# Kernel optimization log

Hardware: AMD Instinct MI355X
Metric: run time of the kernel (lower is better)

## Reference

```python
import jax, jax.numpy as jnp
import numpy as np

EMB = 1024
HID = 2048
NH = 16
NKV = 16
NE = 8
TOPK = 2
WIN = 2048
B = 2
L = 2048
HD = EMB // NH  # 64


def _layer_norm(x, g, b, eps=1e-5):
    m = jnp.mean(x, axis=-1, keepdims=True)
    v = jnp.mean((x - m) ** 2, axis=-1, keepdims=True)
    return (x - m) / jnp.sqrt(v + eps) * g + b


def setup_inputs() -> dict:
    key = jax.random.key(0)
    ks = jax.random.split(key, 12)
    w = lambda k, shape: (jax.random.normal(k, shape, jnp.float32) * 0.02)
    return {
        "x": jax.random.normal(ks[0], (B, L, EMB), jnp.float32),
        "position_idx": 0,
        "ln1_g": jnp.ones((EMB,), jnp.float32),
        "ln1_b": jnp.zeros((EMB,), jnp.float32),
        "ln2_g": jnp.ones((EMB,), jnp.float32),
        "ln2_b": jnp.zeros((EMB,), jnp.float32),
        "Wq": w(ks[1], (EMB, EMB)),
        "Wk": w(ks[2], (EMB, EMB)),
        "Wv": w(ks[3], (EMB, EMB)),
        "Wo": w(ks[4], (EMB, EMB)),
        "Wr": w(ks[5], (EMB, NE)),
        "W1": w(ks[6], (NE, EMB, HID)),
        "b1": jnp.zeros((NE, HID), jnp.float32),
        "W2": w(ks[7], (NE, HID, EMB)),
        "b2": jnp.zeros((NE, EMB), jnp.float32),
    }


def reference(x, position_idx, ln1_g, ln1_b, ln2_g, ln2_b, Wq, Wk, Wv, Wo, Wr, W1, b1, W2, b2):
    Bn, Ln, D = x.shape
    scale = 1.0 / (HD ** 0.5)

    # --- sliding-window attention (cache=None path) ---
    h = _layer_norm(x, ln1_g, ln1_b)
    q = (h @ Wq).reshape(Bn, Ln, NH, HD).transpose(0, 2, 1, 3)   # [B,H,L,hd]
    k = (h @ Wk).reshape(Bn, Ln, NKV, HD).transpose(0, 2, 1, 3)  # [B,KV,L,hd]
    v = (h @ Wv).reshape(Bn, Ln, NKV, HD).transpose(0, 2, 1, 3)
    k = k[:, :, -WIN:]
    v = v[:, :, -WIN:]
    qpk = NH // NKV
    if qpk > 1:
        k = jnp.repeat(k, qpk, axis=1)
        v = jnp.repeat(v, qpk, axis=1)
    scores = jnp.einsum('bhqd,bhkd->bhqk', q, k) * scale
    S = k.shape[2]
    i = jnp.arange(Ln)[:, None]
    j = jnp.arange(S)[None, :]
    mask = (j > i) | (j < i + position_idx - WIN)  # causal + sliding window
    scores = jnp.where(mask[None, None], -jnp.inf, scores)
    attn = jax.nn.softmax(scores, axis=-1)
    attn_out = jnp.einsum('bhqk,bhkd->bqhd', attn, v).reshape(Bn, Ln, D) @ Wo
    x = x + attn_out

    # --- top-k MoE ---
    h2 = _layer_norm(x, ln2_g, ln2_b)
    logits = h2 @ Wr                               # [B,L,E]
    top_v, top_i = jax.lax.top_k(logits, TOPK)     # [B,L,K]
    top_w = jax.nn.softmax(top_v, axis=-1)
    out = jnp.zeros_like(x)
    for e in range(NE):
        # combine weight for expert e per token (sums over top-k slots)
        we = jnp.sum(jnp.where(top_i == e, top_w, 0.0), axis=-1)  # [B,L]
        he = jax.nn.silu(h2 @ W1[e] + b1[e])
        out = out + we[..., None] * (he @ W2[e] + b2[e])
    return x + out
```

## Files before the change

### kernel.cpp

```cpp
#include <hip/hip_runtime.h>
#include <hip/hip_bf16.h>

typedef __hip_bfloat16 bf16;
typedef __attribute__((ext_vector_type(8))) short bf16x8;
typedef __attribute__((ext_vector_type(4))) float f32x4;

constexpr int kEMB = 1024;
constexpr int kHID = 2048;
constexpr int kNH  = 16;
constexpr int kNE  = 8;
constexpr int kL   = 2048;
constexpr int kHD  = 64;
constexpr int kT   = 4096;
constexpr int kSLOTS = kT * 2;
constexpr int kWIN = 2048;

__device__ __forceinline__ unsigned short f2bfbits(float f){
  bf16 h = __float2bfloat16(f);
  return __builtin_bit_cast(unsigned short, h);
}
__device__ __forceinline__ float bfbits2f(unsigned short u){
  unsigned int x = ((unsigned int)u) << 16;
  return __builtin_bit_cast(float, x);
}
__device__ __forceinline__ void gld_lds16(const void* g, void* s){
  __builtin_amdgcn_global_load_lds((const __attribute__((address_space(1))) void*)g,
                                   (__attribute__((address_space(3))) void*)s, 16, 0, 0);
}
__device__ __forceinline__ float wave_sum64(float v){
  #pragma unroll
  for (int xm = 1; xm < 64; xm <<= 1) v += __shfl_xor(v, xm, 64);
  return v;
}

__global__ __launch_bounds__(256) void tconv_k(const float* __restrict__ src, bf16* __restrict__ dst,
                                               int R, int C){
  __shared__ float tile[32][33];
  const int tx = threadIdx.x & 31, ty = threadIdx.x >> 5;
  const int bx = blockIdx.x * 32, by = blockIdx.y * 32;
  const size_t base = (size_t)blockIdx.z * R * C;
  #pragma unroll
  for (int i = 0; i < 32; i += 8)
    tile[ty + i][tx] = src[base + (size_t)(by + ty + i) * C + bx + tx];
  __syncthreads();
  #pragma unroll
  for (int i = 0; i < 32; i += 8)
    dst[base + (size_t)(bx + ty + i) * R + by + tx] = __float2bfloat16(tile[tx][ty + i]);
}

__global__ __launch_bounds__(256) void tconv4_k(const float* __restrict__ s0, const float* __restrict__ s1,
                                                const float* __restrict__ s2, const float* __restrict__ s3,
                                                bf16* __restrict__ dst){
  __shared__ float tile[32][33];
  const int tx = threadIdx.x & 31, ty = threadIdx.x >> 5;
  const int bx = blockIdx.x * 32, by = blockIdx.y * 32;
  const int z = blockIdx.z;
  const float* src = (z == 0) ? s0 : (z == 1) ? s1 : (z == 2) ? s2 : s3;
  bf16* d = dst + (size_t)z * kEMB * kEMB;
  #pragma unroll
  for (int i = 0; i < 32; i += 8)
    tile[ty + i][tx] = src[(size_t)(by + ty + i) * kEMB + bx + tx];
  __syncthreads();
  #pragma unroll
  for (int i = 0; i < 32; i += 8)
    d[(size_t)(bx + ty + i) * kEMB + by + tx] = __float2bfloat16(tile[tx][ty + i]);
}

__global__ __launch_bounds__(256) void vtrans_k(const bf16* __restrict__ v, bf16* __restrict__ vt){
  __shared__ unsigned short tile[32][33];
  const int tx = threadIdx.x & 31, ty = threadIdx.x >> 5;
  const int l0 = blockIdx.x * 32, d0 = blockIdx.y * 32;
  const unsigned short* src = (const unsigned short*)v + (size_t)blockIdx.z * kL * kHD;
  unsigned short* dst = (unsigned short*)vt + (size_t)blockIdx.z * kHD * kL;
  #pragma unroll
  for (int i = 0; i < 32; i += 8)
    tile[ty + i][tx] = src[(size_t)(l0 + ty + i) * kHD + d0 + tx];
  __syncthreads();
  #pragma unroll
  for (int i = 0; i < 32; i += 8)
    dst[(size_t)(d0 + ty + i) * kL + l0 + tx] = tile[tx][ty + i];
}

__global__ __launch_bounds__(256) void lnw_k(
    const float* __restrict__ x, const float* __restrict__ g, const float* __restrict__ bta,
    bf16* __restrict__ h)
{
  const int lane = threadIdx.x & 63, w = threadIdx.x >> 6;
  const int row = blockIdx.x * 4 + w;
  const float4* xr = (const float4*)(x + (size_t)row * kEMB);
  float4 v[4];
  #pragma unroll
  for (int j = 0; j < 4; j++) v[j] = xr[lane + 64 * j];
  float s = 0.f;
  #pragma unroll
  for (int j = 0; j < 4; j++) s += v[j].x + v[j].y + v[j].z + v[j].w;
  s = wave_sum64(s);
  const float mean = s * (1.0f / kEMB);
  float ss = 0.f;
  #pragma unroll
  for (int j = 0; j < 4; j++){
    const float a = v[j].x - mean, b = v[j].y - mean, c = v[j].z - mean, d = v[j].w - mean;
    ss += a*a + b*b + c*c + d*d;
  }
  ss = wave_sum64(ss);
  const float rstd = rsqrtf(ss * (1.0f / kEMB) + 1e-5f);
  unsigned short* hr = (unsigned short*)h + (size_t)row * kEMB;
  #pragma unroll
  for (int j = 0; j < 4; j++){
    const float4 gg = ((const float4*)g)[lane + 64 * j];
    const float4 bb = ((const float4*)bta)[lane + 64 * j];
    ushort4 pk;
    pk.x = f2bfbits((v[j].x - mean) * rstd * gg.x + bb.x);
    pk.y = f2bfbits((v[j].y - mean) * rstd * gg.y + bb.y);
    pk.z = f2bfbits((v[j].z - mean) * rstd * gg.z + bb.z);
    pk.w = f2bfbits((v[j].w - mean) * rstd * gg.w + bb.w);
    *(ushort4*)&hr[(lane + 64 * j) * 4] = pk;
  }
}

__global__ __launch_bounds__(256) void ln2w_k(
    const float* __restrict__ x, const float* __restrict__ P,
    const float* __restrict__ g, const float* __restrict__ bta,
    float* __restrict__ out, bf16* __restrict__ h, const float* __restrict__ Wr,
    int* __restrict__ top_i, float* __restrict__ top_w)
{
  const int lane = threadIdx.x & 63, w = threadIdx.x >> 6;
  const int row = blockIdx.x * 4 + w;
  const float4* xr = (const float4*)(x + (size_t)row * kEMB);
  const float4* p0 = (const float4*)(P + (size_t)row * kEMB);
  const float4* p1 = (const float4*)(P + (size_t)(kT + row) * kEMB);
  float4* outr = (float4*)(out + (size_t)row * kEMB);
  float4 v[4];
  #pragma unroll
  for (int j = 0; j < 4; j++){
    const float4 a = xr[lane + 64 * j], b = p0[lane + 64 * j], c = p1[lane + 64 * j];
    v[j].x = a.x + b.x + c.x; v[j].y = a.y + b.y + c.y;
    v[j].z = a.z + b.z + c.z; v[j].w = a.w + b.w + c.w;
    outr[lane + 64 * j] = v[j];
  }
  float s = 0.f;
  #pragma unroll
  for (int j = 0; j < 4; j++) s += v[j].x + v[j].y + v[j].z + v[j].w;
  s = wave_sum64(s);
  const float mean = s * (1.0f / kEMB);
  float ss = 0.f;
  #pragma unroll
  for (int j = 0; j < 4; j++){
    const float a = v[j].x - mean, b = v[j].y - mean, c = v[j].z - mean, d = v[j].w - mean;
    ss += a*a + b*b + c*c + d*d;
  }
  ss = wave_sum64(ss);
  const float rstd = rsqrtf(ss * (1.0f / kEMB) + 1e-5f);
  unsigned short* hr = (unsigned short*)h + (size_t)row * kEMB;
  float part[8];
  #pragma unroll
  for (int e = 0; e < 8; e++) part[e] = 0.f;
  #pragma unroll
  for (int j = 0; j < 4; j++){
    const float4 gg = ((const float4*)g)[lane + 64 * j];
    const float4 bb = ((const float4*)bta)[lane + 64 * j];
    float n[4];
    n[0] = (v[j].x - mean) * rstd * gg.x + bb.x;
    n[1] = (v[j].y - mean) * rstd * gg.y + bb.y;
    n[2] = (v[j].z - mean) * rstd * gg.z + bb.z;
    n[3] = (v[j].w - mean) * rstd * gg.w + bb.w;
    ushort4 pk;
    pk.x = f2bfbits(n[0]); pk.y = f2bfbits(n[1]); pk.z = f2bfbits(n[2]); pk.w = f2bfbits(n[3]);
    *(ushort4*)&hr[(lane + 64 * j) * 4] = pk;
    const float* wrp = Wr + (size_t)(lane + 64 * j) * 4 * kNE;
    #pragma unroll
    for (int i = 0; i < 4; i++)
      #pragma unroll
      for (int e = 0; e < 8; e++) part[e] += n[i] * wrp[i * kNE + e];
  }
  #pragma unroll
  for (int xm = 1; xm < 64; xm <<= 1)
    #pragma unroll
    for (int e = 0; e < 8; e++) part[e] += __shfl_xor(part[e], xm, 64);
  if (lane == 0){
    int i0 = 0; float v0 = part[0];
    #pragma unroll
    for (int e = 1; e < 8; e++) if (part[e] > v0){ v0 = part[e]; i0 = e; }
    int i1 = -1; float v1 = -3.4e38f;
    #pragma unroll
    for (int e = 0; e < 8; e++) if (e != i0 && part[e] > v1){ v1 = part[e]; i1 = e; }
    const float w0 = 1.0f / (1.0f + __expf(v1 - v0));
    top_i[row * 2] = i0; top_i[row * 2 + 1] = i1;
    top_w[row * 2] = w0; top_w[row * 2 + 1] = 1.0f - w0;
  }
}

template<int MODE>
__global__ __launch_bounds__(256) void gemm_k(
    const bf16* __restrict__ A, const bf16* __restrict__ BT, int K,
    float* __restrict__ fdst, bf16* __restrict__ bdst)
{
  __shared__ alignas(16) unsigned short As[2][128 * 64];
  __shared__ alignas(16) unsigned short Bs[2][128 * 64];
  const int tid = threadIdx.x, lane = tid & 63, w = tid >> 6;
  const int wr = w >> 1, wc = w & 1;
  const int bx = blockIdx.x, by = blockIdx.y;
  int kt0 = 0, nkt = K / 64;
  if (MODE == 1){ kt0 = blockIdx.z * (K / 2); nkt = K / 128; }
  const int m0 = by * 128, n0 = bx * 128;
  f32x4 acc[4][4] = {};
  const int srow = lane >> 3;
  const int skk  = (lane & 7) * 8;

  auto stage = [&](int t, int buf){
    const int kt = kt0 + t * 64;
    #pragma unroll
    for (int j = 0; j < 4; j++){
      const int rr = w * 32 + j * 8;
      gld_lds16(A + (size_t)(m0 + rr + srow) * K + kt + skk, &As[buf][rr * 64]);
      gld_lds16(BT + (size_t)(n0 + rr + srow) * K + kt + skk, &Bs[buf][rr * 64]);
    }
  };

  stage(0, 0);
  __syncthreads();
  for (int t = 0; t < nkt; t++){
    const int cur = t & 1;
    if (t + 1 < nkt) stage(t + 1, cur ^ 1);
    #pragma unroll
    for (int ks = 0; ks < 2; ks++){
      bf16x8 af[4], bfm[4];
      #pragma unroll
      for (int i = 0; i < 4; i++){
        af[i]  = *(const bf16x8*)&As[cur][(wr * 64 + i * 16 + (lane & 15)) * 64 + ks * 32 + (lane >> 4) * 8];
        bfm[i] = *(const bf16x8*)&Bs[cur][(wc * 64 + i * 16 + (lane & 15)) * 64 + ks * 32 + (lane >> 4) * 8];
      }
      #pragma unroll
      for (int i = 0; i < 4; i++)
        #pragma unroll
        for (int j = 0; j < 4; j++)
          acc[i][j] = __builtin_amdgcn_mfma_f32_16x16x32_bf16(af[i], bfm[j], acc[i][j], 0, 0, 0);
    }
    __syncthreads();
  }

  #pragma unroll
  for (int i = 0; i < 4; i++){
    #pragma unroll
    for (int r = 0; r < 4; r++){
      const int gm = m0 + wr * 64 + i * 16 + (lane >> 4) * 4 + r;
      if (MODE == 1){
        float* pdst = fdst + (size_t)blockIdx.z * kT * kEMB;
        #pragma unroll
        for (int jn = 0; jn < 4; jn++){
          const int gn = n0 + wc * 64 + jn * 16 + (lane & 15);
          pdst[(size_t)gm * kEMB + gn] = acc[i][jn][r];
        }
      } else {
        const int bidx = gm >> 11, l = gm & (kL - 1);
        #pragma unroll
        for (int jn = 0; jn < 4; jn++){
          const int gn = n0 + wc * 64 + jn * 16 + (lane & 15);
          const int sec = gn >> 10;
          const int nn = gn & 1023;
          const int hh = nn >> 6, d = nn & 63;
          const float val = acc[i][jn][r] * (sec == 0 ? 0.18033688f : 1.0f);
          bdst[(size_t)sec * kT * kEMB + (((size_t)bidx * kNH + hh) * kL + l) * kHD + d] =
              __float2bfloat16(val);
        }
      }
    }
  }
}

template<int MODE>
__global__ __launch_bounds__(256, 4) void gemm3_k(
    const bf16* __restrict__ A, const bf16* __restrict__ BT, int K,
    bf16* __restrict__ bdst, const float* __restrict__ bias,
    const float* __restrict__ roww, const int* __restrict__ rowtok,
    const int* __restrict__ offs)
{
  __shared__ alignas(16) unsigned short As[3][128 * 32];
  __shared__ alignas(16) unsigned short Bs[2][128 * 32];
  const int tid = threadIdx.x, lane = tid & 63, w = tid >> 6;
  const int wr = w >> 1, wc = w & 1;
  const int e = blockIdx.x & 7, s = blockIdx.x >> 3;
  const int bx = (MODE == 2) ? (s & 15) : (s & 7);
  const int by = (MODE == 2) ? (s >> 4) : (s >> 3);
  const int rbase = offs[e], rend = offs[e + 1];
  if (by * 128 >= rend - rbase) return;
  const int m0 = by * 128, n0 = bx * 128;
  const int NB = (MODE == 2) ? kHID : kEMB;
  const bf16* Bp = BT + (size_t)e * NB * K;
  const float* biasp = bias + e * NB;
  const int nkt = K / 32;
  f32x4 acc[4][4] = {};

  const int sc = tid & 3, sr0 = tid >> 2;
  const int scs = (sc ^ (sr0 & 3)) * 8;
  size_t aoffs[2]; size_t boffs[2];
  {
    int p0 = rbase + m0 + sr0;      if (p0 >= rend) p0 = rbase;
    int p1 = rbase + m0 + 64 + sr0; if (p1 >= rend) p1 = rbase;
    aoffs[0] = (size_t)((MODE == 2) ? rowtok[p0] : p0) * K;
    aoffs[1] = (size_t)((MODE == 2) ? rowtok[p1] : p1) * K;
    boffs[0] = (size_t)(n0 + sr0) * K;
    boffs[1] = (size_t)(n0 + 64 + sr0) * K;
  }

  auto stageA = [&](int t){
    const int b = t % 3; const int kt = t * 32;
    gld_lds16(A + aoffs[0] + kt + scs, &As[b][tid * 8]);
    gld_lds16(A + aoffs[1] + kt + scs, &As[b][(tid + 256) * 8]);
  };
  auto stageB = [&](int t){
    const int b = t & 1; const int kt = t * 32;
    gld_lds16(Bp + boffs[0] + kt + scs, &Bs[b][tid * 8]);
    gld_lds16(Bp + boffs[1] + kt + scs, &Bs[b][(tid + 256) * 8]);
  };

  stageB(0);
  stageA(0);
  if (nkt > 1) stageA(1);
  asm volatile("s_waitcnt vmcnt(0)" ::: "memory");
  __builtin_amdgcn_s_barrier();

  for (int t = 0; t < nkt; t++){
    if (t > 0){
      if (t + 1 < nkt) { asm volatile("s_waitcnt vmcnt(2)" ::: "memory"); }
      else             { asm volatile("s_waitcnt vmcnt(0)" ::: "memory"); }
      __builtin_amdgcn_s_barrier();
    }
    const int ca = t % 3, cb = t & 1;
    bf16x8 af[4], bfm[4];
    const int cc = lane >> 4;
    #pragma unroll
    for (int i = 0; i < 4; i++){
      const int ar = wr * 64 + i * 16 + (lane & 15);
      af[i] = *(const bf16x8*)&As[ca][ar * 32 + ((cc ^ (ar & 3)) * 8)];
    }
    #pragma unroll
    for (int j = 0; j < 4; j++){
      const int br = wc * 64 + j * 16 + (lane & 15);
      bfm[j] = *(const bf16x8*)&Bs[cb][br * 32 + ((cc ^ (br & 3)) * 8)];
    }
    __builtin_amdgcn_s_setprio(1);
    #pragma unroll
    for (int i = 0; i < 4; i++)
      #pragma unroll
      for (int j = 0; j < 4; j++)
        acc[i][j] = __builtin_amdgcn_mfma_f32_16x16x32_bf16(af[i], bfm[j], acc[i][j], 0, 0, 0);
    __builtin_amdgcn_s_setprio(0);
    if (t + 1 < nkt) stageB(t + 1);
    if (t + 2 < nkt) stageA(t + 2);
  }

  #pragma unroll
  for (int i = 0; i < 4; i++){
    #pragma unroll
    for (int r = 0; r < 4; r++){
      const int p = rbase + m0 + wr * 64 + i * 16 + (lane >> 4) * 4 + r;
      if (p < rend){
        if (MODE == 2){
          #pragma unroll
          for (int jn = 0; jn < 4; jn++){
            const int gn = n0 + wc * 64 + jn * 16 + (lane & 15);
            const float vv = acc[i][jn][r] + biasp[gn];
            bdst[(size_t)p * NB + gn] = __float2bfloat16(vv / (1.0f + __expf(-vv)));
          }
        } else {
          const float wgt = roww[p];
          #pragma unroll
          for (int jn = 0; jn < 4; jn++){
            const int gn = n0 + wc * 64 + jn * 16 + (lane & 15);
            bdst[(size_t)p * NB + gn] = __float2bfloat16((acc[i][jn][r] + biasp[gn]) * wgt);
          }
        }
      }
    }
  }
}

__global__ __launch_bounds__(256) void attn_k(
    const bf16* __restrict__ q, const bf16* __restrict__ k, const bf16* __restrict__ vt,
    bf16* __restrict__ o, const int* __restrict__ pos)
{
  const int bid = blockIdx.x;
  const int qt = 31 - (bid >> 5);
  const int bh = bid & 31;
  const int tid = threadIdx.x, lane = tid & 63, w = tid >> 6;
  const unsigned short* qp  = (const unsigned short*)q  + (size_t)bh * kL * kHD;
  const unsigned short* kp  = (const unsigned short*)k  + (size_t)bh * kL * kHD;
  const unsigned short* vtp = (const unsigned short*)vt + (size_t)bh * kHD * kL;
  __shared__ alignas(16) unsigned short Ks[2][64 * 64];
  __shared__ alignas(16) unsigned short Vt[2][64 * 64];
  __shared__ alignas(16) unsigned short pl[4 * 16 * 72];
  const int q0 = qt * 64 + w * 16;
  const int pos0 = pos[0];
  const int wlo = pos0 - kWIN;

  bf16x8 qf[2];
  {
    const int qrow = q0 + (lane & 15);
    #pragma unroll
    for (int ks = 0; ks < 2; ks++)
      qf[ks] = *(const bf16x8*)&qp[(size_t)qrow * kHD + ks * 32 + (lane >> 4) * 8];
  }
  float m_run[4], l_part[4];
  f32x4 oacc[4] = {};
  #pragma unroll
  for (int r = 0; r < 4; r++){ m_run[r] = -1e30f; l_part[r] = 0.f; }

  auto stage = [&](int kt, int buf){
    #pragma unroll
    for (int j = 0; j < 2; j++){
      const int r = w * 16 + j * 8 + (lane >> 3);
      const int c = (lane & 7) ^ (r & 7);
      gld_lds16(kp  + (size_t)(kt * 64 + r) * 64 + c * 8, &Ks[buf][(w * 16 + j * 8) * 64]);
      gld_lds16(vtp + (size_t)r * kL + kt * 64 + c * 8,   &Vt[buf][(w * 16 + j * 8) * 64]);
    }
  };

  stage(0, 0);
  for (int kt = 0; kt <= qt; kt++){
    const int buf = kt & 1;
    __syncthreads();
    if (kt < qt) stage(kt + 1, buf ^ 1);

    f32x4 s[4];
    #pragma unroll
    for (int kbk = 0; kbk < 4; kbk++){
      const int row = kbk * 16 + (lane & 15);
      f32x4 a = {0.f, 0.f, 0.f, 0.f};
      #pragma unroll
      for (int ks = 0; ks < 2; ks++){
        const int chnk = ks * 4 + (lane >> 4);
        const bf16x8 kf = *(const bf16x8*)&Ks[buf][row * 64 + ((chnk ^ (row & 7)) * 8)];
        a = __builtin_amdgcn_mfma_f32_16x16x32_bf16(qf[ks], kf, a, 0, 0, 0);
      }
      s[kbk] = a;
    }
    const bool needmask = (kt == qt) || (kt * 64 < q0 + 16 + wlo);
    if (needmask){
      #pragma unroll
      for (int kbk = 0; kbk < 4; kbk++){
        const int j = kt * 64 + kbk * 16 + (lane & 15);
        #pragma unroll
        for (int r = 0; r < 4; r++){
          const int i = q0 + (lane >> 4) * 4 + r;
          if (j > i || j < i + wlo) s[kbk][r] = -1e30f;
        }
      }
    }
    float pmax[4];
    #pragma unroll
    for (int r = 0; r < 4; r++) pmax[r] = s[0][r];
    #pragma unroll
    for (int kbk = 1; kbk < 4; kbk++)
      #pragma unroll
      for (int r = 0; r < 4; r++) pmax[r] = fmaxf(pmax[r], s[kbk][r]);
    bool need = false;
    #pragma unroll
    for (int r = 0; r < 4; r++) need |= (pmax[r] > m_run[r] + 8.0f);
    if (__any(need)){
      float tm[4];
      #pragma unroll
      for (int r = 0; r < 4; r++) tm[r] = pmax[r];
      #pragma unroll
      for (int xm = 1; xm < 16; xm <<= 1)
        #pragma unroll
        for (int r = 0; r < 4; r++) tm[r] = fmaxf(tm[r], __shfl_xor(tm[r], xm, 64));
      #pragma unroll
      for (int r = 0; r < 4; r++){
        const float mn = fmaxf(m_run[r], tm[r]);
        const float corr = exp2f(m_run[r] - mn);
        m_run[r] = mn;
        l_part[r] *= corr;
        #pragma unroll
        for (int db = 0; db < 4; db++) oacc[db][r] *= corr;
      }
    }
    #pragma unroll
    for (int kbk = 0; kbk < 4; kbk++)
      #pragma unroll
      for (int r = 0; r < 4; r++){
        const float p = exp2f(s[kbk][r] - m_run[r]);
        s[kbk][r] = p;
        l_part[r] += p;
      }
    #pragma unroll
    for (int kbk = 0; kbk < 4; kbk++)
      #pragma unroll
      for (int r = 0; r < 4; r++)
        pl[(w * 16 + (lane >> 4) * 4 + r) * 72 + kbk * 16 + (lane & 15)] = f2bfbits(s[kbk][r]);
    asm volatile("s_waitcnt lgkmcnt(0)" ::: "memory");
    __builtin_amdgcn_sched_barrier(0);
    bf16x8 pa[2];
    #pragma unroll
    for (int ks = 0; ks < 2; ks++)
      pa[ks] = *(const bf16x8*)&pl[(w * 16 + (lane & 15)) * 72 + ks * 32 + (lane >> 4) * 8];
    #pragma unroll
    for (int db = 0; db < 4; db++){
      const int row = db * 16 + (lane & 15);
      #pragma unroll
      for (int ks = 0; ks < 2; ks++){
        const int chnk = ks * 4 + (lane >> 4);
        const bf16x8 vf = *(const bf16x8*)&Vt[buf][row * 64 + ((chnk ^ (row & 7)) * 8)];
        oacc[db] = __builtin_amdgcn_mfma_f32_16x16x32_bf16(pa[ks], vf, oacc[db], 0, 0, 0);
      }
    }
  }
  #pragma unroll
  for (int xm = 1; xm < 16; xm <<= 1)
    #pragma unroll
    for (int r = 0; r < 4; r++) l_part[r] += __shfl_xor(l_part[r], xm, 64);
  const int hh = bh & (kNH - 1), bidx = bh >> 4;
  #pragma unroll
  for (int db = 0; db < 4; db++){
    #pragma unroll
    for (int r = 0; r < 4; r++){
      const int i = q0 + (lane >> 4) * 4 + r;
      const int d = db * 16 + (lane & 15);
      o[((size_t)(bidx * kL + i)) * kEMB + hh * kHD + d] = __float2bfloat16(oacc[db][r] / l_part[r]);
    }
  }
}

__global__ void zero_k(int* counts){ if (threadIdx.x < kNE) counts[threadIdx.x] = 0; }

__global__ __launch_bounds__(256) void count_k(const int* __restrict__ top_i, int* __restrict__ counts){
  const int idx = blockIdx.x * 256 + threadIdx.x;
  if (idx < kSLOTS) atomicAdd(&counts[top_i[idx]], 1);
}

__global__ void scan_k(const int* __restrict__ counts, int* __restrict__ offs, int* __restrict__ cursor){
  int o = 0;
  for (int e = 0; e < kNE; e++){ offs[e] = o; cursor[e] = o; o += counts[e]; }
  offs[kNE] = o;
}

__global__ __launch_bounds__(256) void assign_k(const int* __restrict__ top_i, const float* __restrict__ top_w,
                                                int* __restrict__ cursor, int* __restrict__ rowtok,
                                                float* __restrict__ roww, int* __restrict__ tok2row){
  const int idx = blockIdx.x * 256 + threadIdx.x;
  if (idx < kSLOTS){
    const int e = top_i[idx];
    const int p = atomicAdd(&cursor[e], 1);
    rowtok[p] = idx >> 1;
    roww[p] = top_w[idx];
    tok2row[idx] = p;
  }
}

__global__ __launch_bounds__(256) void combine_k(float* __restrict__ out, const bf16* __restrict__ g2,
                                                 const int* __restrict__ tok2row){
  const int t = blockIdx.x, c = threadIdx.x * 4;
  const int r0 = tok2row[t * 2], r1 = tok2row[t * 2 + 1];
  const ushort4 ua = *(const ushort4*)((const unsigned short*)g2 + (size_t)r0 * kEMB + c);
  const ushort4 ub = *(const ushort4*)((const unsigned short*)g2 + (size_t)r1 * kEMB + c);
  float* op = out + (size_t)t * kEMB + c;
  float4 ov = *(float4*)op;
  ov.x += bfbits2f(ua.x) + bfbits2f(ub.x);
  ov.y += bfbits2f(ua.y) + bfbits2f(ub.y);
  ov.z += bfbits2f(ua.z) + bfbits2f(ub.z);
  ov.w += bfbits2f(ua.w) + bfbits2f(ub.w);
  *(float4*)op = ov;
}

extern "C" void kernel_launch(void* const* d_in, const int* in_sizes, int n_in,
                              void* d_out, int out_size, void* d_ws, size_t ws_size,
                              hipStream_t stream)
{
  const float* x    = (const float*)d_in[0];
  const int*   pos  = (const int*)d_in[1];
  const float* ln1g = (const float*)d_in[2];
  const float* ln1b = (const float*)d_in[3];
  const float* ln2g = (const float*)d_in[4];
  const float* ln2b = (const float*)d_in[5];
  const float* Wq   = (const float*)d_in[6];
  const float* Wk   = (const float*)d_in[7];
  const float* Wv   = (const float*)d_in[8];
  const float* Wo   = (const float*)d_in[9];
  const float* Wr   = (const float*)d_in[10];
  const float* W1   = (const float*)d_in[11];
  const float* b1   = (const float*)d_in[12];
  const float* W2   = (const float*)d_in[13];
  const float* b2   = (const float*)d_in[14];
  float* out = (float*)d_out;

  char* p = (char*)d_ws;
  auto alloc = [&](size_t bytes) -> char* {
    char* r = p; p += (bytes + 255) & ~(size_t)255; return r;
  };
  bf16* WqkvT = (bf16*)alloc((size_t)3 * kEMB * kEMB * 2);
  bf16* WoT   = (bf16*)alloc((size_t)kEMB * kEMB * 2);
  bf16* W1T   = (bf16*)alloc((size_t)kNE * kEMB * kHID * 2);
  bf16* W2T   = (bf16*)alloc((size_t)kNE * kEMB * kHID * 2);
  bf16* hbf   = (bf16*)alloc((size_t)kT * kEMB * 2);
  bf16* qkv   = (bf16*)alloc((size_t)3 * kT * kEMB * 2);
  bf16* vtbf  = (bf16*)alloc((size_t)kT * kEMB * 2);
  bf16* abf   = (bf16*)alloc((size_t)kT * kEMB * 2);
  bf16* h2bf  = (bf16*)alloc((size_t)kT * kEMB * 2);
  bf16* hebf  = (bf16*)alloc((size_t)kSLOTS * kHID * 2);
  bf16* g2bf  = (bf16*)alloc((size_t)kSLOTS * kEMB * 2);
  int*   top_i   = (int*)alloc(kSLOTS * 4);
  float* top_w   = (float*)alloc(kSLOTS * 4);
  int*   counts  = (int*)alloc(64);
  int*   offs    = (int*)alloc(64);
  int*   cursor  = (int*)alloc(64);
  int*   rowtok  = (int*)alloc(kSLOTS * 4);
  float* rowwgt  = (float*)alloc(kSLOTS * 4);
  int*   tok2row = (int*)alloc(kSLOTS * 4);
  bf16* qbf = qkv;
  bf16* kbf = qkv + (size_t)kT * kEMB;
  bf16* vbf = qkv + (size_t)2 * kT * kEMB;
  float* Pws = (float*)hbf;
  (void)in_sizes; (void)n_in; (void)out_size; (void)ws_size;

  tconv4_k<<<dim3(32, 32, 4), 256, 0, stream>>>(Wq, Wk, Wv, Wo, WqkvT);
  tconv_k<<<dim3(64, 32, kNE), 256, 0, stream>>>(W1, W1T, kEMB, kHID);
  tconv_k<<<dim3(32, 64, kNE), 256, 0, stream>>>(W2, W2T, kHID, kEMB);

  lnw_k<<<kT / 4, 256, 0, stream>>>(x, ln1g, ln1b, hbf);

  gemm_k<4><<<dim3(24, 32), 256, 0, stream>>>(hbf, WqkvT, kEMB, nullptr, qkv);

  vtrans_k<<<dim3(kL / 32, kHD / 32, 32), 256, 0, stream>>>(vbf, vtbf);

  attn_k<<<dim3(1024), 256, 0, stream>>>(qbf, kbf, vtbf, abf, pos);

  gemm_k<1><<<dim3(8, 32, 2), 256, 0, stream>>>(abf, WoT, kEMB, Pws, nullptr);

  ln2w_k<<<kT / 4, 256, 0, stream>>>(x, Pws, ln2g, ln2b, out, h2bf, Wr, top_i, top_w);

  zero_k<<<1, 64, 0, stream>>>(counts);
  count_k<<<kSLOTS / 256, 256, 0, stream>>>(top_i, counts);
  scan_k<<<1, 1, 0, stream>>>(counts, offs, cursor);
  assign_k<<<kSLOTS / 256, 256, 0, stream>>>(top_i, top_w, cursor, rowtok, rowwgt, tok2row);

  gemm3_k<2><<<dim3(8 * 32 * 16), 256, 0, stream>>>(h2bf, W1T, kEMB, hebf, b1, nullptr, rowtok, offs);
  gemm3_k<3><<<dim3(8 * 32 * 8), 256, 0, stream>>>(hebf, W2T, kHID, g2bf, b2, rowwgt, nullptr, offs);

  combine_k<<<kT, 256, 0, stream>>>(out, g2bf, tok2row);
}
```

Before: 369.0 us.

## Split-K the second expert GEMM and merge histogram kernels into one

The down-projection expert GEMM is split along K into two halves, each writing a separate bf16 partial buffer. The combine kernel sums both partials per token, and bias is added only by the first half. This doubles the block count of the under-filled GEMM to raise occupancy, at the cost of extra partial-output traffic and bf16 rounding of each partial. The zero/count/scan kernels are also replaced by a single-block shared-memory histogram kernel, which removes two launches.

```diff
diff --git a/kernel.cpp b/kernel.cpp
--- a/kernel.cpp
+++ b/kernel.cpp
@@ -271,7 +271,7 @@
 template<int MODE>
 __global__ __launch_bounds__(256, 4) void gemm3_k(
     const bf16* __restrict__ A, const bf16* __restrict__ BT, int K,
-    bf16* __restrict__ bdst, const float* __restrict__ bias,
+    bf16* __restrict__ bdst, bf16* __restrict__ bdstB, const float* __restrict__ bias,
     const float* __restrict__ roww, const int* __restrict__ rowtok,
     const int* __restrict__ offs)
 {
@@ -279,16 +279,21 @@
   __shared__ alignas(16) unsigned short Bs[2][128 * 32];
   const int tid = threadIdx.x, lane = tid & 63, w = tid >> 6;
   const int wr = w >> 1, wc = w & 1;
-  const int e = blockIdx.x & 7, s = blockIdx.x >> 3;
-  const int bx = (MODE == 2) ? (s & 15) : (s & 7);
-  const int by = (MODE == 2) ? (s >> 4) : (s >> 3);
+  int e, bx, by, half = 0;
+  if (MODE == 2){
+    e = blockIdx.x & 7; const int s = blockIdx.x >> 3; by = s >> 4; bx = s & 15;
+  } else {
+    e = blockIdx.x & 7; half = (blockIdx.x >> 3) & 1;
+    const int s2 = blockIdx.x >> 4; bx = s2 & 7; by = s2 >> 3;
+  }
   const int rbase = offs[e], rend = offs[e + 1];
   if (by * 128 >= rend - rbase) return;
   const int m0 = by * 128, n0 = bx * 128;
   const int NB = (MODE == 2) ? kHID : kEMB;
   const bf16* Bp = BT + (size_t)e * NB * K;
   const float* biasp = bias + e * NB;
-  const int nkt = K / 32;
+  const int kt0 = (MODE == 3) ? half * (K / 2) : 0;
+  const int nkt = ((MODE == 3) ? K / 2 : K) / 32;
   f32x4 acc[4][4] = {};
 
   const int sc = tid & 3, sr0 = tid >> 2;
@@ -304,12 +309,12 @@
   }
 
   auto stageA = [&](int t){
-    const int b = t % 3; const int kt = t * 32;
+    const int b = t % 3; const int kt = kt0 + t * 32;
     gld_lds16(A + aoffs[0] + kt + scs, &As[b][tid * 8]);
     gld_lds16(A + aoffs[1] + kt + scs, &As[b][(tid + 256) * 8]);
   };
   auto stageB = [&](int t){
-    const int b = t & 1; const int kt = t * 32;
+    const int b = t & 1; const int kt = kt0 + t * 32;
     gld_lds16(Bp + boffs[0] + kt + scs, &Bs[b][tid * 8]);
     gld_lds16(Bp + boffs[1] + kt + scs, &Bs[b][(tid + 256) * 8]);
   };
@@ -361,14 +366,16 @@
           for (int jn = 0; jn < 4; jn++){
             const int gn = n0 + wc * 64 + jn * 16 + (lane & 15);
             const float vv = acc[i][jn][r] + biasp[gn];
-            bdst[(size_t)p * NB + gn] = __float2bfloat16(vv / (1.0f + __expf(-vv)));
+            bdst[(size_t)p * kHID + gn] = __float2bfloat16(vv / (1.0f + __expf(-vv)));
           }
         } else {
           const float wgt = roww[p];
+          bf16* dst = half ? bdstB : bdst;
           #pragma unroll
           for (int jn = 0; jn < 4; jn++){
             const int gn = n0 + wc * 64 + jn * 16 + (lane & 15);
-            bdst[(size_t)p * NB + gn] = __float2bfloat16((acc[i][jn][r] + biasp[gn]) * wgt);
+            const float bb = half ? 0.f : biasp[gn];
+            dst[(size_t)p * kEMB + gn] = __float2bfloat16((acc[i][jn][r] + bb) * wgt);
           }
         }
       }
@@ -521,17 +528,17 @@
   }
 }
 
-__global__ void zero_k(int* counts){ if (threadIdx.x < kNE) counts[threadIdx.x] = 0; }
-
-__global__ __launch_bounds__(256) void count_k(const int* __restrict__ top_i, int* __restrict__ counts){
-  const int idx = blockIdx.x * 256 + threadIdx.x;
-  if (idx < kSLOTS) atomicAdd(&counts[top_i[idx]], 1);
-}
-
-__global__ void scan_k(const int* __restrict__ counts, int* __restrict__ offs, int* __restrict__ cursor){
-  int o = 0;
-  for (int e = 0; e < kNE; e++){ offs[e] = o; cursor[e] = o; o += counts[e]; }
-  offs[kNE] = o;
+__global__ void hist_k(const int* __restrict__ top_i, int* __restrict__ offs, int* __restrict__ cursor){
+  __shared__ int lc[kNE];
+  if (threadIdx.x < kNE) lc[threadIdx.x] = 0;
+  __syncthreads();
+  for (int i = threadIdx.x; i < kSLOTS; i += 256) atomicAdd(&lc[top_i[i]], 1);
+  __syncthreads();
+  if (threadIdx.x == 0){
+    int o = 0;
+    for (int e = 0; e < kNE; e++){ offs[e] = o; cursor[e] = o; o += lc[e]; }
+    offs[kNE] = o;
+  }
 }
 
 __global__ __launch_bounds__(256) void assign_k(const int* __restrict__ top_i, const float* __restrict__ top_w,
@@ -548,17 +555,20 @@
 }
 
 __global__ __launch_bounds__(256) void combine_k(float* __restrict__ out, const bf16* __restrict__ g2,
+                                                 const bf16* __restrict__ g2b,
                                                  const int* __restrict__ tok2row){
   const int t = blockIdx.x, c = threadIdx.x * 4;
   const int r0 = tok2row[t * 2], r1 = tok2row[t * 2 + 1];
-  const ushort4 ua = *(const ushort4*)((const unsigned short*)g2 + (size_t)r0 * kEMB + c);
-  const ushort4 ub = *(const ushort4*)((const unsigned short*)g2 + (size_t)r1 * kEMB + c);
+  const ushort4 ua = *(const ushort4*)((const unsigned short*)g2  + (size_t)r0 * kEMB + c);
+  const ushort4 ub = *(const ushort4*)((const unsigned short*)g2  + (size_t)r1 * kEMB + c);
+  const ushort4 uc = *(const ushort4*)((const unsigned short*)g2b + (size_t)r0 * kEMB + c);
+  const ushort4 ud = *(const ushort4*)((const unsigned short*)g2b + (size_t)r1 * kEMB + c);
   float* op = out + (size_t)t * kEMB + c;
   float4 ov = *(float4*)op;
-  ov.x += bfbits2f(ua.x) + bfbits2f(ub.x);
-  ov.y += bfbits2f(ua.y) + bfbits2f(ub.y);
-  ov.z += bfbits2f(ua.z) + bfbits2f(ub.z);
-  ov.w += bfbits2f(ua.w) + bfbits2f(ub.w);
+  ov.x += bfbits2f(ua.x) + bfbits2f(ub.x) + bfbits2f(uc.x) + bfbits2f(ud.x);
+  ov.y += bfbits2f(ua.y) + bfbits2f(ub.y) + bfbits2f(uc.y) + bfbits2f(ud.y);
+  ov.z += bfbits2f(ua.z) + bfbits2f(ub.z) + bfbits2f(uc.z) + bfbits2f(ud.z);
+  ov.w += bfbits2f(ua.w) + bfbits2f(ub.w) + bfbits2f(uc.w) + bfbits2f(ud.w);
   *(float4*)op = ov;
 }
 
@@ -600,7 +610,6 @@
   bf16* g2bf  = (bf16*)alloc((size_t)kSLOTS * kEMB * 2);
   int*   top_i   = (int*)alloc(kSLOTS * 4);
   float* top_w   = (float*)alloc(kSLOTS * 4);
-  int*   counts  = (int*)alloc(64);
   int*   offs    = (int*)alloc(64);
   int*   cursor  = (int*)alloc(64);
   int*   rowtok  = (int*)alloc(kSLOTS * 4);
@@ -610,6 +619,7 @@
   bf16* kbf = qkv + (size_t)kT * kEMB;
   bf16* vbf = qkv + (size_t)2 * kT * kEMB;
   float* Pws = (float*)hbf;
+  bf16* g2bf2 = (bf16*)hbf;
   (void)in_sizes; (void)n_in; (void)out_size; (void)ws_size;
 
   tconv4_k<<<dim3(32, 32, 4), 256, 0, stream>>>(Wq, Wk, Wv, Wo, WqkvT);
@@ -628,13 +638,11 @@
 
   ln2w_k<<<kT / 4, 256, 0, stream>>>(x, Pws, ln2g, ln2b, out, h2bf, Wr, top_i, top_w);
 
-  zero_k<<<1, 64, 0, stream>>>(counts);
-  count_k<<<kSLOTS / 256, 256, 0, stream>>>(top_i, counts);
-  scan_k<<<1, 1, 0, stream>>>(counts, offs, cursor);
+  hist_k<<<1, 256, 0, stream>>>(top_i, offs, cursor);
   assign_k<<<kSLOTS / 256, 256, 0, stream>>>(top_i, top_w, cursor, rowtok, rowwgt, tok2row);
 
-  gemm3_k<2><<<dim3(8 * 32 * 16), 256, 0, stream>>>(h2bf, W1T, kEMB, hebf, b1, nullptr, rowtok, offs);
-  gemm3_k<3><<<dim3(8 * 32 * 8), 256, 0, stream>>>(hebf, W2T, kHID, g2bf, b2, rowwgt, nullptr, offs);
-
-  combine_k<<<kT, 256, 0, stream>>>(out, g2bf, tok2row);
-}
+  gemm3_k<2><<<dim3(8 * 32 * 16), 256, 0, stream>>>(h2bf, W1T, kEMB, hebf, nullptr, b1, nullptr, rowtok, offs);
+  gemm3_k<3><<<dim3(8 * 2 * 8 * 32), 256, 0, stream>>>(hebf, W2T, kHID, g2bf, g2bf2, b2, rowwgt, nullptr, offs);
+
+  combine_k<<<kT, 256, 0, stream>>>(out, g2bf, g2bf2, tok2row);
+}
```

New measurement: 373.7 us. Within noise of the previous version (+1.3%).
